# Kernel tuning notes

Hardware: AMD Instinct MI355X
Metric: run time of the kernel (lower is better)

## Reference

```python
import jax, jax.numpy as jnp
import numpy as np

BATCH, LENGTH, HIDDEN, SSM = 32, 2048, 128, 256


def setup_inputs() -> dict:
    key = jax.random.key(0)
    ks = jax.random.split(key, 7)
    b_std = 1.0 / np.sqrt(HIDDEN)
    c_std = 1.0 / np.sqrt(SSM)
    return {
        "inputs": jax.random.normal(ks[0], (BATCH, LENGTH, HIDDEN), jnp.float32),
        "A_diag": jax.random.normal(ks[1], (SSM,), jnp.float32),
        "G_diag": jax.random.uniform(ks[2], (SSM,), jnp.float32),
        "steps": jax.random.normal(ks[3], (SSM,), jnp.float32) * 0.5,
        "B": jax.random.uniform(ks[4], (SSM, HIDDEN, 2), jnp.float32, -b_std, b_std),
        "C": jax.random.uniform(ks[5], (HIDDEN, SSM, 2), jnp.float32, -c_std, c_std),
        "D": jax.random.normal(ks[6], (HIDDEN,), jnp.float32),
    }


def _project_parameters(A_diag, G_diag, steps):
    # Mirrors DampedLinOSSLayer._project_parameters: sigmoid step, relu damping,
    # and clamp A into the band where the 2x2 IMEX1 transition has complex eigenvalues.
    step = jax.nn.sigmoid(steps)
    g = jax.nn.relu(G_diag)
    denom = jnp.maximum(step * step, 1e-6)
    s = step * g
    base = jnp.sqrt(jnp.maximum(1.0 + s, 1e-6))
    a_low = (2.0 + s - 2.0 * base) / denom
    a_high = (2.0 + s + 2.0 * base) / denom
    a = a_low + jax.nn.relu(A_diag - a_low) - jax.nn.relu(A_diag - a_high)
    return a, g, step


def _eigenvalue(a, g, step):
    # IMEX1 transition M = [[S, -S*dt*A], [dt*S, 1 - dt^2*S*A]] with S = 1/(1+dt*G).
    # det(M) = S, trace(M) = S + 1 - dt^2*S*A; projection guarantees trace^2 < 4*det,
    # so eigenvalues form a conjugate pair lam = T/2 + i*sqrt(S - T^2/4).
    S = 1.0 / (1.0 + step * g)
    T = S + 1.0 - step * step * S * a
    imag = jnp.sqrt(jnp.maximum(S - 0.25 * T * T, 0.0))
    return jax.lax.complex(0.5 * T, imag)  # [P] complex64


def reference(inputs, A_diag, G_diag, steps, B, C, D):
    a, g, step = _project_parameters(A_diag, G_diag, steps)
    lam = _eigenvalue(a, g, step)  # [P]

    # Complex input projection: bu = (B_re + i*B_im) @ u, shape [batch, L, P]
    bu = jax.lax.complex(
        jnp.einsum("blh,ph->blp", inputs, B[..., 0]),
        jnp.einsum("blh,ph->blp", inputs, B[..., 1]),
    )

    # Diagonal complex linear recurrence x_k = lam * x_{k-1} + bu_k via associative scan.
    def combine(e1, e2):
        a1, b1 = e1
        a2, b2 = e2
        return a1 * a2, a2 * b1 + b2

    lam_b = jnp.broadcast_to(lam[None, None, :], bu.shape)
    _, states = jax.lax.associative_scan(combine, (lam_b, bu), axis=1)

    # Output: Re(C @ x) + D * u
    projected = (
        jnp.einsum("blp,hp->blh", states.real, C[..., 0])
        - jnp.einsum("blp,hp->blh", states.imag, C[..., 1])
    )
    return projected + inputs * D
```

## Files before the change

kernel.cpp:

```cpp
#include <hip/hip_runtime.h>
#include <hip/hip_bf16.h>
#include <math.h>

#define BATCH 32
#define LEN   2048
#define HID   128
#define SSM   256

#define BPL 32768

typedef __attribute__((ext_vector_type(4))) float f32x4;
typedef __attribute__((ext_vector_type(8))) short bf16x8;
typedef __attribute__((ext_vector_type(4))) int   i32x4;

static __device__ __forceinline__ unsigned short f2bf(float x) {
    union { float f; unsigned u; } v; v.f = x;
    unsigned r = (v.u + 0x7FFFu + ((v.u >> 16) & 1u)) >> 16;
    return (unsigned short)r;
}
static __device__ __forceinline__ unsigned short f2bf_hi(float x) {
    union { float f; unsigned u; } v; v.f = x;
    return (unsigned short)(v.u >> 16);
}
static __device__ __forceinline__ float bf2f(unsigned short b) {
    union { unsigned u; float f; } v; v.u = ((unsigned)b) << 16;
    return v.f;
}
static __device__ __forceinline__ unsigned int cvtpk(float a, float b) {
    __hip_bfloat162 h = __float22bfloat162_rn(float2{a, b});
    union { __hip_bfloat162 h2; unsigned int u; } c; c.h2 = h;
    return c.u;
}
static __device__ __forceinline__ void cmul(float& rr, float& ri,
                                            float ar, float ai, float br, float bi) {
    rr = ar * br - ai * bi;
    ri = ar * bi + ai * br;
}
static __device__ __forceinline__ void gload16(const void* g, void* l) {
    __builtin_amdgcn_global_load_lds(
        (const __attribute__((address_space(1))) unsigned int*)g,
        (__attribute__((address_space(3))) unsigned int*)l,
        16, 0, 0);
}

__global__ __launch_bounds__(256) void k0b_prep(const float* __restrict__ Bm,
                                                const float* __restrict__ Cm,
                                                const float* __restrict__ A,
                                                const float* __restrict__ G,
                                                const float* __restrict__ steps,
                                                unsigned short* __restrict__ Bsp,
                                                unsigned short* __restrict__ C2,
                                                float* __restrict__ lam) {
    if (blockIdx.x == 256) {
        int p = threadIdx.x;
        if (p < SSM) {
            float stp   = 1.f / (1.f + expf(-steps[p]));
            float g     = fmaxf(G[p], 0.f);
            float denom = fmaxf(stp * stp, 1e-6f);
            float s     = stp * g;
            float base  = sqrtf(fmaxf(1.f + s, 1e-6f));
            float alow  = (2.f + s - 2.f * base) / denom;
            float ahigh = (2.f + s + 2.f * base) / denom;
            float a     = alow + fmaxf(A[p] - alow, 0.f) - fmaxf(A[p] - ahigh, 0.f);
            float S     = 1.f / (1.f + stp * g);
            float T     = S + 1.f - stp * stp * S * a;
            lam[p]       = 0.5f * T;
            lam[SSM + p] = sqrtf(fmaxf(S - 0.25f * T * T, 0.f));
        }
        return;
    }
    int gidx = blockIdx.x * 256 + threadIdx.x;
    if (gidx < 32768) {
        int p = gidx >> 7, h = gidx & 127;
        float vr = Bm[(size_t)(p * HID + h) * 2];
        float vi = Bm[(size_t)(p * HID + h) * 2 + 1];
        unsigned short hh = f2bf_hi(vr);
        Bsp[0 * BPL + p * HID + h] = hh;
        Bsp[1 * BPL + p * HID + h] = f2bf(vr - bf2f(hh));
        hh = f2bf_hi(vi);
        Bsp[2 * BPL + p * HID + h] = hh;
        Bsp[3 * BPL + p * HID + h] = f2bf(vi - bf2f(hh));
    } else {
        int g2 = gidx - 32768;
        int h = g2 >> 8, p = g2 & 255;
        float vr = Cm[(size_t)(h * SSM + p) * 2];
        float vi = -Cm[(size_t)(h * SSM + p) * 2 + 1];
        unsigned short rh = f2bf_hi(vr);
        unsigned short ih = f2bf_hi(vi);
        size_t rowh = (size_t)h * 512;
        C2[rowh + 2 * p]               = rh;
        C2[rowh + 2 * p + 1]           = ih;
        C2[65536 + rowh + 2 * p]       = f2bf(vr - bf2f(rh));
        C2[65536 + rowh + 2 * p + 1]   = f2bf(vi - bf2f(ih));
    }
}

__global__ __launch_bounds__(256) void ku_cvt(const float* __restrict__ u,
                                              unsigned short* __restrict__ ubf) {
    const int total = BATCH * LEN * HID;
    const int stride = 2048 * 256 * 8;
    for (int i = (blockIdx.x * 256 + threadIdx.x) * 8; i < total; i += stride) {
        f32x4 a = *(const f32x4*)&u[i];
        f32x4 c = *(const f32x4*)&u[i + 4];
        i32x4 o;
        o[0] = (int)cvtpk(a[0], a[1]);
        o[1] = (int)cvtpk(a[2], a[3]);
        o[2] = (int)cvtpk(c[0], c[1]);
        o[3] = (int)cvtpk(c[2], c[3]);
        *(i32x4*)&ubf[i] = o;
    }
}

__global__ __launch_bounds__(512, 4) void k12_fused(const unsigned short* __restrict__ ubf,
                                                    const unsigned short* __restrict__ Bsp,
                                                    const float* __restrict__ lam,
                                                    unsigned short* __restrict__ TP) {
    __shared__ __align__(16) char sU[2][32768];
    __shared__ __align__(16) char sT2[10240];
    __shared__ float Rld[4][2][8][2];

    int d    = blockIdx.x;
    int xcd  = d & 7;
    int idx  = d >> 3;
    int pt   = idx & 15;
    int bhi  = idx >> 4;
    int b    = bhi * 8 + xcd;
    int p0   = pt * 16;

    int tid  = threadIdx.x;
    int lane = tid & 63, w = tid >> 6;
    int wl   = w >> 1, wp = w & 1;
    int fr   = lane & 15, g = lane >> 4;
    int frp  = fr & 7;
    int comp = fr >> 3;
    int pcol = p0 + wp * 8 + frp;

    const unsigned short* Bh  = Bsp + (size_t)(comp * 2) * BPL + (size_t)pcol * HID;
    const unsigned short* Blo = Bsp + (size_t)(comp * 2 + 1) * BPL + (size_t)pcol * HID;
    bf16x8 Bfh[4], Bfl[4];
#pragma unroll
    for (int kc = 0; kc < 4; ++kc) {
        Bfh[kc] = *(const bf16x8*)&Bh[kc * 32 + g * 8];
        Bfl[kc] = *(const bf16x8*)&Blo[kc * 32 + g * 8];
    }

    float pw_r[4], pw_i[4];
    float lg_r, lg_i;
    float l4r, l4i, l8r, l8i, l16r, l16i, l32r, l32i;
    {
        float ar = lam[pcol], ai = lam[SSM + pcol];
        pw_r[0] = ar; pw_i[0] = ai;
        cmul(pw_r[1], pw_i[1], ar, ai, ar, ai);
        cmul(pw_r[2], pw_i[2], pw_r[1], pw_i[1], ar, ai);
        cmul(pw_r[3], pw_i[3], pw_r[1], pw_i[1], pw_r[1], pw_i[1]);
        l4r = pw_r[3]; l4i = pw_i[3];
        cmul(l8r, l8i, l4r, l4i, l4r, l4i);
        cmul(l16r, l16i, l8r, l8i, l8r, l8i);
        cmul(l32r, l32i, l16r, l16i, l16r, l16i);
        if (g == 0)      { lg_r = 1.f; lg_i = 0.f; }
        else if (g == 1) { lg_r = l4r; lg_i = l4i; }
        else if (g == 2) { lg_r = l8r; lg_i = l8i; }
        else             { cmul(lg_r, lg_i, l8r, l8i, l4r, l4i); }
    }

    float TCr = 0.f, TCi = 0.f;

    const unsigned short* ub = ubf + (size_t)b * (LEN * HID);
    int srow32  = tid >> 4;
    int stg_src = srow32 * HID + ((((tid & 15) * 16) ^ ((srow32 & 7) << 4)) >> 1);

#define STAGE(buf, tt)                                                        \
    {                                                                         \
        const unsigned short* gs = ub + (size_t)(tt) * 16384 + stg_src;       \
        char* ls = &sU[buf][tid * 16];                                        \
        _Pragma("unroll")                                                     \
        for (int q = 0; q < 4; ++q)                                           \
            gload16(gs + q * 4096, ls + q * 8192);                            \
    }

    STAGE(0, 0)
    __syncthreads();
    int cur = 0;

    for (int t = 0; t < 16; ++t) {
        int l0t = t * 128;

        if (t < 15) STAGE(cur ^ 1, t + 1)

        const char* su = &sU[cur][0];
        f32x4 acc[2];
        acc[0] = (f32x4)(0.f); acc[1] = (f32x4)(0.f);
#pragma unroll
        for (int kc = 0; kc < 4; ++kc) {
#pragma unroll
            for (int mi = 0; mi < 2; ++mi) {
                int off = (wl * 32 + mi * 16 + fr) * 256 + ((kc * 64 + g * 16) ^ ((fr & 7) << 4));
                bf16x8 ah = *(const bf16x8*)(su + off);
                acc[mi] = __builtin_amdgcn_mfma_f32_16x16x32_bf16(ah, Bfh[kc], acc[mi], 0, 0, 0);
                acc[mi] = __builtin_amdgcn_mfma_f32_16x16x32_bf16(ah, Bfl[kc], acc[mi], 0, 0, 0);
            }
        }

        float xr[4], xi[4];
#pragma unroll
        for (int e = 0; e < 4; ++e) {
            float send = (comp == 0) ? acc[1][e] : acc[0][e];
            float oth  = __shfl_xor(send, 8, 64);
            xr[e] = (comp == 0) ? acc[0][e] : oth;
            xi[e] = (comp == 0) ? oth       : acc[1][e];
        }

        float Er, Ei, Fr, Fi, For, Foi;
        {
            float lr = pw_r[0], li = pw_i[0];
            float cr = 0.f, ci = 0.f;
#pragma unroll
            for (int r = 0; r < 4; ++r) {
                float nr = fmaf(lr, cr, fmaf(-li, ci, xr[r]));
                float ni = fmaf(lr, ci, fmaf(li, cr, xi[r]));
                cr = nr; ci = ni;
                xr[r] = cr; xi[r] = ci;
            }
            float Qr = cr, Qi = ci;
            float ur = __shfl_up(Qr, 16u, 64);
            float ui = __shfl_up(Qi, 16u, 64);
            if (g >= 1) {
                Qr = fmaf(l4r, ur, fmaf(-l4i, ui, Qr));
                Qi = fmaf(l4r, ui, fmaf(l4i, ur, Qi));
            }
            ur = __shfl_up(Qr, 32u, 64);
            ui = __shfl_up(Qi, 32u, 64);
            if (g >= 2) {
                Qr = fmaf(l8r, ur, fmaf(-l8i, ui, Qr));
                Qi = fmaf(l8r, ui, fmaf(l8i, ur, Qi));
            }
            Er = __shfl_up(Qr, 16u, 64);
            Ei = __shfl_up(Qi, 16u, 64);
            if (g == 0) { Er = 0.f; Ei = 0.f; }
            Fr = __shfl(Qr, fr + 48, 64);
            Fi = __shfl(Qi, fr + 48, 64);
            For = __shfl_xor(Fr, 8, 64);
            Foi = __shfl_xor(Fi, 8, 64);
            float Rr = fmaf(l16r, For, fmaf(-l16i, Foi, Fr));
            float Ri = fmaf(l16r, Foi, fmaf(l16i, For, Fi));
            if (g == 0 && fr >= 8) { Rld[wl][wp][frp][0] = Rr; Rld[wl][wp][frp][1] = Ri; }
        }
        __syncthreads();

        {
            float Wr = TCr, Wi = TCi;
            float Tr = TCr, Ti = TCi;
#pragma unroll
            for (int w2 = 0; w2 < 4; ++w2) {
                float rr = Rld[w2][wp][frp][0], ri = Rld[w2][wp][frp][1];
                float nTr = fmaf(l32r, Tr, fmaf(-l32i, Ti, rr));
                float nTi = fmaf(l32r, Ti, fmaf(l32i, Tr, ri));
                Tr = nTr; Ti = nTi;
                if (w2 < wl) {
                    float nWr = fmaf(l32r, Wr, fmaf(-l32i, Wi, rr));
                    float nWi = fmaf(l32r, Wi, fmaf(l32i, Wr, ri));
                    Wr = nWr; Wi = nWi;
                }
            }
            TCr = Tr; TCi = Ti;
            float prr, pri;
            if (comp == 0) { prr = Wr; pri = Wi; }
            else {
                prr = fmaf(l16r, Wr, fmaf(-l16i, Wi, For));
                pri = fmaf(l16r, Wi, fmaf(l16i, Wr, Foi));
            }
            float Mr = fmaf(lg_r, prr, fmaf(-lg_i, pri, Er));
            float Mi = fmaf(lg_r, pri, fmaf(lg_i, prr, Ei));
#pragma unroll
            for (int r = 0; r < 4; ++r) {
                xr[r] = fmaf(pw_r[r], Mr, fmaf(-pw_i[r], Mi, xr[r]));
                xi[r] = fmaf(pw_r[r], Mi, fmaf(pw_i[r], Mr, xi[r]));
            }
        }

        {
            int colb  = wl * 32 + comp * 16 + g * 4;
            int idxu  = wp * 8 + frp;
            int piece = idxu >> 2, sub = idxu & 3;
            int pw    = piece ^ g;
#pragma unroll
            for (int r = 0; r < 4; ++r) {
                unsigned int pk = cvtpk(xr[r], xi[r]);
                *(unsigned int*)(sT2 + (colb + r) * 80 + pw * 16 + sub * 4) = pk;
            }
        }
        __syncthreads();

        {
            int row = tid >> 2, q = tid & 3;
            int x2  = (row >> 2) & 3;
            bf16x8 v = *(const bf16x8*)(sT2 + row * 80 + ((q ^ x2) * 16));
            *(bf16x8*)&TP[((size_t)(b * LEN) + l0t + row) * 512 + p0 * 2 + q * 8] = v;
        }
        cur ^= 1;
    }
#undef STAGE
}

__global__ __launch_bounds__(512, 4) void k3_out(const unsigned short* __restrict__ TP,
                                                 const unsigned short* __restrict__ C2,
                                                 const unsigned short* __restrict__ ubf,
                                                 const float* __restrict__ D,
                                                 float* __restrict__ out) {
    __shared__ __align__(16) char sAB[2][24576];

    int d    = blockIdx.x;
    int xcd  = d & 7;
    int rest = d >> 3;
    int lt   = rest & 15;
    int bhi  = rest >> 4;
    int b    = bhi * 8 + xcd;
    int l0   = lt * 128;

    int tid = threadIdx.x;
    int lane = tid & 63, w = tid >> 6;
    int wl = w >> 1, wh = w & 1;
    int fr = lane & 15, g = lane >> 4;

    f32x4 acc[2][4];
#pragma unroll
    for (int mi = 0; mi < 2; ++mi)
#pragma unroll
        for (int ni = 0; ni < 4; ++ni) acc[mi][ni] = (f32x4)(0.f);

    float dv[4];
#pragma unroll
    for (int ni = 0; ni < 4; ++ni) dv[ni] = D[wh * 64 + ni * 16 + fr];

#define STAGE3(buf, cc)                                                       \
    {                                                                         \
                                                  \
        {                                                                     \
            int rw = tid >> 2, sl = tid & 3;                                  \
            gload16(TP + ((size_t)(b * LEN) + l0 + rw) * 512 + (cc) * 32 +    \
                        ((sl ^ (rw & 3)) * 8),                                \
                    &sAB[buf][tid * 16]);                                     \
        }                                                                     \
                                             \
        _Pragma("unroll")                                                     \
        for (int q = 0; q < 2; ++q) {                                         \
            int dg = tid + q * 512;                                           \
            int hl = dg >> 9, hr = (dg >> 2) & 127, sl = dg & 3;              \
            gload16(C2 + ((size_t)(hl * 128 + hr)) * 512 + (cc) * 32 +        \
                        ((sl ^ (hr & 3)) * 8),                                \
                    &sAB[buf][8192 + dg * 16]);                               \
        }                                                                     \
    }

    STAGE3(0, 0)
    __syncthreads();
    int cur = 0;

    for (int c = 0; c < 16; ++c) {
        if (c < 15) STAGE3(cur ^ 1, c + 1)

        const char* sb = &sAB[cur][0];
        int swz = (g ^ (fr & 3)) * 16;
        bf16x8 af[2];
#pragma unroll
        for (int mi = 0; mi < 2; ++mi) {
            int arow = wl * 32 + mi * 16 + fr;
            af[mi] = *(const bf16x8*)(sb + arow * 64 + swz);
        }
#pragma unroll
        for (int ni = 0; ni < 4; ++ni) {
            int hrow = wh * 64 + ni * 16 + fr;
            bf16x8 ch = *(const bf16x8*)(sb + 8192 + hrow * 64 + swz);
            bf16x8 cl = *(const bf16x8*)(sb + 8192 + 8192 + hrow * 64 + swz);
#pragma unroll
            for (int mi = 0; mi < 2; ++mi) {
                acc[mi][ni] = __builtin_amdgcn_mfma_f32_16x16x32_bf16(af[mi], ch, acc[mi][ni], 0, 0, 0);
                acc[mi][ni] = __builtin_amdgcn_mfma_f32_16x16x32_bf16(af[mi], cl, acc[mi][ni], 0, 0, 0);
            }
        }
        __syncthreads();
        cur ^= 1;
    }
#undef STAGE3

#pragma unroll
    for (int mi = 0; mi < 2; ++mi)
#pragma unroll
        for (int ni = 0; ni < 4; ++ni) {
            int lb = l0 + wl * 32 + mi * 16 + g * 4;
            int h  = wh * 64 + ni * 16 + fr;
#pragma unroll
            for (int r = 0; r < 4; ++r) {
                size_t idx = ((size_t)b * LEN + lb + r) * HID + h;
                out[idx] = acc[mi][ni][r] + bf2f(ubf[idx]) * dv[ni];
            }
        }
}

extern "C" void kernel_launch(void* const* d_in, const int* in_sizes, int n_in,
                              void* d_out, int out_size, void* d_ws, size_t ws_size,
                              hipStream_t stream) {
    const float* u  = (const float*)d_in[0];
    const float* A  = (const float*)d_in[1];
    const float* G  = (const float*)d_in[2];
    const float* st = (const float*)d_in[3];
    const float* B  = (const float*)d_in[4];
    const float* C  = (const float*)d_in[5];
    const float* D  = (const float*)d_in[6];
    float* out = (float*)d_out;

    char* WS = (char*)d_ws;
    unsigned short* TP  = (unsigned short*)WS;
    float* lam          = (float*)(WS + 67108864);
    unsigned short* Bsp = (unsigned short*)(WS + 67110912);
    unsigned short* C2  = (unsigned short*)(WS + 67373056);
    unsigned short* ubf = (unsigned short*)(WS + 67635200);

    k0b_prep<<<257, 256, 0, stream>>>(B, C, A, G, st, Bsp, C2, lam);
    ku_cvt<<<2048, 256, 0, stream>>>(u, ubf);
    k12_fused<<<512, 512, 0, stream>>>(ubf, Bsp, lam, TP);
    k3_out<<<512, 512, 0, stream>>>(TP, C2, ubf, D, out);
}
```

Baseline: 86.44 us.

## Merge prep kernels, triple-buffer output GEMM loads, and relax barrier waits

Merges the u-to-bf16 conversion and the parameter prep into one launch, so one kernel launch and its gap go away. The output GEMM kernel moves from double to triple buffering of LDS tiles and prefetches two stages ahead. Its full __syncthreads is replaced by a partial vmcnt wait plus s_barrier, so global loads for later stages can stay in flight across the barrier. The fused scan kernel likewise swaps __syncthreads for an explicit lgkmcnt wait and barrier. The cost is extra LDS per block in k3_out, which may reduce occupancy, and hand-tuned waitcnt values that must match the number of outstanding loads.

Result: faster. 81.71 us (-5.5%).

```diff
diff --git a/kernel.cpp b/kernel.cpp
--- a/kernel.cpp
+++ b/kernel.cpp
@@ -43,15 +43,32 @@
         16, 0, 0);
 }
 
-__global__ __launch_bounds__(256) void k0b_prep(const float* __restrict__ Bm,
-                                                const float* __restrict__ Cm,
-                                                const float* __restrict__ A,
-                                                const float* __restrict__ G,
-                                                const float* __restrict__ steps,
-                                                unsigned short* __restrict__ Bsp,
-                                                unsigned short* __restrict__ C2,
-                                                float* __restrict__ lam) {
-    if (blockIdx.x == 256) {
+__global__ __launch_bounds__(256) void kprep(const float* __restrict__ u,
+                                             const float* __restrict__ Bm,
+                                             const float* __restrict__ Cm,
+                                             const float* __restrict__ A,
+                                             const float* __restrict__ G,
+                                             const float* __restrict__ steps,
+                                             unsigned short* __restrict__ ubf,
+                                             unsigned short* __restrict__ Bsp,
+                                             unsigned short* __restrict__ C2,
+                                             float* __restrict__ lam) {
+    if (blockIdx.x < 2048) {
+        const int total = BATCH * LEN * HID;
+        const int stride = 2048 * 256 * 8;
+        for (int i = (blockIdx.x * 256 + threadIdx.x) * 8; i < total; i += stride) {
+            f32x4 a = *(const f32x4*)&u[i];
+            f32x4 c = *(const f32x4*)&u[i + 4];
+            i32x4 o;
+            o[0] = (int)cvtpk(a[0], a[1]);
+            o[1] = (int)cvtpk(a[2], a[3]);
+            o[2] = (int)cvtpk(c[0], c[1]);
+            o[3] = (int)cvtpk(c[2], c[3]);
+            *(i32x4*)&ubf[i] = o;
+        }
+        return;
+    }
+    if (blockIdx.x == 2304) {
         int p = threadIdx.x;
         if (p < SSM) {
             float stp   = 1.f / (1.f + expf(-steps[p]));
@@ -69,7 +86,7 @@
         }
         return;
     }
-    int gidx = blockIdx.x * 256 + threadIdx.x;
+    int gidx = (blockIdx.x - 2048) * 256 + threadIdx.x;
     if (gidx < 32768) {
         int p = gidx >> 7, h = gidx & 127;
         float vr = Bm[(size_t)(p * HID + h) * 2];
@@ -95,22 +112,6 @@
     }
 }
 
-__global__ __launch_bounds__(256) void ku_cvt(const float* __restrict__ u,
-                                              unsigned short* __restrict__ ubf) {
-    const int total = BATCH * LEN * HID;
-    const int stride = 2048 * 256 * 8;
-    for (int i = (blockIdx.x * 256 + threadIdx.x) * 8; i < total; i += stride) {
-        f32x4 a = *(const f32x4*)&u[i];
-        f32x4 c = *(const f32x4*)&u[i + 4];
-        i32x4 o;
-        o[0] = (int)cvtpk(a[0], a[1]);
-        o[1] = (int)cvtpk(a[2], a[3]);
-        o[2] = (int)cvtpk(c[0], c[1]);
-        o[3] = (int)cvtpk(c[2], c[3]);
-        *(i32x4*)&ubf[i] = o;
-    }
-}
-
 __global__ __launch_bounds__(512, 4) void k12_fused(const unsigned short* __restrict__ ubf,
                                                     const unsigned short* __restrict__ Bsp,
                                                     const float* __restrict__ lam,
@@ -245,7 +246,9 @@
             float Ri = fmaf(l16r, Foi, fmaf(l16i, For, Fi));
             if (g == 0 && fr >= 8) { Rld[wl][wp][frp][0] = Rr; Rld[wl][wp][frp][1] = Ri; }
         }
-        __syncthreads();
+        asm volatile("s_waitcnt lgkmcnt(0)" ::: "memory");
+        __builtin_amdgcn_s_barrier();
+        __builtin_amdgcn_sched_barrier(0);
 
         {
             float Wr = TCr, Wi = TCi;
@@ -307,7 +310,7 @@
                                                  const unsigned short* __restrict__ ubf,
                                                  const float* __restrict__ D,
                                                  float* __restrict__ out) {
-    __shared__ __align__(16) char sAB[2][24576];
+    __shared__ __align__(16) char sAB[3][24576];
 
     int d    = blockIdx.x;
     int xcd  = d & 7;
@@ -334,14 +337,12 @@
 
 #define STAGE3(buf, cc)                                                       \
     {                                                                         \
-                                                  \
         {                                                                     \
             int rw = tid >> 2, sl = tid & 3;                                  \
             gload16(TP + ((size_t)(b * LEN) + l0 + rw) * 512 + (cc) * 32 +    \
                         ((sl ^ (rw & 3)) * 8),                                \
                     &sAB[buf][tid * 16]);                                     \
         }                                                                     \
-                                             \
         _Pragma("unroll")                                                     \
         for (int q = 0; q < 2; ++q) {                                         \
             int dg = tid + q * 512;                                           \
@@ -354,10 +355,11 @@
 
     STAGE3(0, 0)
     __syncthreads();
+    STAGE3(1, 1)
+
     int cur = 0;
-
     for (int c = 0; c < 16; ++c) {
-        if (c < 15) STAGE3(cur ^ 1, c + 1)
+        if (c < 14) STAGE3((cur + 2) % 3, c + 2)
 
         const char* sb = &sAB[cur][0];
         int swz = (g ^ (fr & 3)) * 16;
@@ -378,8 +380,14 @@
                 acc[mi][ni] = __builtin_amdgcn_mfma_f32_16x16x32_bf16(af[mi], cl, acc[mi][ni], 0, 0, 0);
             }
         }
-        __syncthreads();
-        cur ^= 1;
+        if (c < 14) {
+            asm volatile("s_waitcnt vmcnt(3) lgkmcnt(0)" ::: "memory");
+        } else {
+            asm volatile("s_waitcnt vmcnt(0) lgkmcnt(0)" ::: "memory");
+        }
+        __builtin_amdgcn_s_barrier();
+        __builtin_amdgcn_sched_barrier(0);
+        cur = (cur + 1) % 3;
     }
 #undef STAGE3
 
@@ -416,8 +424,7 @@
     unsigned short* C2  = (unsigned short*)(WS + 67373056);
     unsigned short* ubf = (unsigned short*)(WS + 67635200);
 
-    k0b_prep<<<257, 256, 0, stream>>>(B, C, A, G, st, Bsp, C2, lam);
-    ku_cvt<<<2048, 256, 0, stream>>>(u, ubf);
+    kprep<<<2305, 256, 0, stream>>>(u, B, C, A, G, st, ubf, Bsp, C2, lam);
     k12_fused<<<512, 512, 0, stream>>>(ubf, Bsp, lam, TP);
     k3_out<<<512, 512, 0, stream>>>(TP, C2, ubf, D, out);
 }
```
